# Performance work log

Hardware: AMD Instinct MI355X
Metric: run time of the kernel (lower is better)

## Reference

```python
import jax, jax.numpy as jnp
import numpy as np

DIM = 96
HEADS = 6
WS = 8                      # window_size
OWS = int(WS * 0.5) + WS    # overlap_win_size = 12
PAD = (OWS - WS) // 2       # 2
Dd = Hh = Ww = 24
B = 1
L = Dd * Hh * Ww
MLP_H = DIM * 2
TBL = (WS + OWS - 1) ** 3   # 6859 relative-position-bias entries


def setup_inputs() -> dict:
    key = jax.random.key(0)
    ks = jax.random.split(key, 8)
    def n(k, shape, s=0.02):
        return jax.random.normal(k, shape, jnp.float32) * s
    return {
        "x": jax.random.normal(ks[0], (B, L, DIM), jnp.float32),
        "ln1_w": jnp.ones((DIM,), jnp.float32),
        "ln1_b": jnp.zeros((DIM,), jnp.float32),
        "qkv_w": n(ks[1], (3 * DIM, DIM)),
        "qkv_b": jnp.zeros((3 * DIM,), jnp.float32),
        "rpb": n(ks[2], (TBL, HEADS)),
        "proj_w": n(ks[3], (DIM, DIM)),
        "proj_b": jnp.zeros((DIM,), jnp.float32),
        "ln2_w": jnp.ones((DIM,), jnp.float32),
        "ln2_b": jnp.zeros((DIM,), jnp.float32),
        "fc1_w": n(ks[4], (MLP_H, DIM)),
        "fc1_b": jnp.zeros((MLP_H,), jnp.float32),
        "fc2_w": n(ks[5], (DIM, MLP_H)),
        "fc2_b": jnp.zeros((DIM,), jnp.float32),
        "rpi": jax.random.randint(ks[6], (WS ** 3, OWS ** 3), 0, TBL),
        "D": Dd, "H": Hh, "W": Ww,
    }


def _ln(x, w, b):
    m = jnp.mean(x, -1, keepdims=True)
    v = jnp.var(x, -1, keepdims=True)
    return (x - m) / jnp.sqrt(v + 1e-5) * w + b


def _ocab3d(x, ln1_w, ln1_b, qkv_w, qkv_b, rpb, proj_w, proj_b,
            ln2_w, ln2_b, fc1_w, fc1_b, fc2_w, fc2_b, rpi, D, H, W):
    Bz, Lz, C = x.shape
    hd = C // HEADS
    scale = hd ** -0.5
    shortcut = x

    xn = _ln(x, ln1_w, ln1_b).reshape(Bz, D, H, W, C)
    qkv = xn @ qkv_w.T + qkv_b                   # [B,D,H,W,3C]
    q = qkv[..., :C]
    kv = qkv[..., C:]                            # cat(k, v) on channels, [B,D,H,W,2C]

    nD, nH, nW = D // WS, H // WS, W // WS
    nw = nD * nH * nW

    # non-overlapping query windows -> [B*nw, WS^3, C]
    qw = q.reshape(Bz, nD, WS, nH, WS, nW, WS, C)
    qw = qw.transpose(0, 1, 3, 5, 2, 4, 6, 7).reshape(Bz * nw, WS ** 3, C)

    # overlapping kv windows via pad + strided gather (mirrors F.pad + unfold)
    kvp = jnp.pad(kv, ((0, 0), (PAD, PAD), (PAD, PAD), (PAD, PAD), (0, 0)))
    idx_d = (jnp.arange(nD) * WS)[:, None] + jnp.arange(OWS)[None, :]
    idx_h = (jnp.arange(nH) * WS)[:, None] + jnp.arange(OWS)[None, :]
    idx_w = (jnp.arange(nW) * WS)[:, None] + jnp.arange(OWS)[None, :]
    kw = kvp[:, idx_d]                 # [B,nD,OWS,Hp,Wp,2C]
    kw = kw[:, :, :, idx_h]            # [B,nD,OWS,nH,OWS,Wp,2C]
    kw = kw[:, :, :, :, :, idx_w]      # [B,nD,OWS,nH,OWS,nW,OWS,2C]
    kw = kw.transpose(0, 1, 3, 5, 2, 4, 6, 7).reshape(Bz * nw, OWS ** 3, 2 * C)
    kk, vv = kw[..., :C], kw[..., C:]

    qh = qw.reshape(-1, WS ** 3, HEADS, hd).transpose(0, 2, 1, 3) * scale
    kh = kk.reshape(-1, OWS ** 3, HEADS, hd).transpose(0, 2, 1, 3)
    vh = vv.reshape(-1, OWS ** 3, HEADS, hd).transpose(0, 2, 1, 3)

    attn = jnp.einsum('bhqd,bhkd->bhqk', qh, kh)               # [B*nw,H,512,1728]
    bias = rpb[rpi.reshape(-1)].reshape(WS ** 3, OWS ** 3, HEADS).transpose(2, 0, 1)
    attn = jax.nn.softmax(attn + bias[None], axis=-1)
    out = jnp.einsum('bhqk,bhkd->bhqd', attn, vh)
    out = out.transpose(0, 2, 1, 3).reshape(Bz * nw, WS ** 3, C)

    # window reverse -> [B, L, C]
    out = out.reshape(Bz, nD, nH, nW, WS, WS, WS, C)
    out = out.transpose(0, 1, 4, 2, 5, 3, 6, 7).reshape(Bz, D * H * W, C)

    x2 = out @ proj_w.T + proj_b + shortcut
    h1 = jax.nn.gelu(_ln(x2, ln2_w, ln2_b) @ fc1_w.T + fc1_b, approximate=False)
    return x2 + (h1 @ fc2_w.T + fc2_b)


def reference(x, ln1_w, ln1_b, qkv_w, qkv_b, rpb, proj_w, proj_b,
              ln2_w, ln2_b, fc1_w, fc1_b, fc2_w, fc2_b, rpi, D, H, W):
    return _ocab3d(x, ln1_w, ln1_b, qkv_w, qkv_b, rpb, proj_w, proj_b,
                   ln2_w, ln2_b, fc1_w, fc1_b, fc2_w, fc2_b, rpi, D, H, W)
```

## Files before the change

kernel.cpp:

```cpp
#include <hip/hip_runtime.h>
#include <math.h>

#define DIMC   96
#define NHEADS 6
#define HD     16
#define WSZ    8
#define OWSZ   12
#define PADW   2
#define DD     24
#define LTOK   13824
#define NWIN   27
#define NKEY   1728
#define NROW   512
#define MLPH   192
#define PDIM   28
#define PD3    21952
#define TBL    6859
#define LSTR   82944
#define AOSTR  1327104
#define LOG2E  1.4426950408889634f

typedef __attribute__((ext_vector_type(4))) short bf16x4;
typedef __attribute__((ext_vector_type(8))) short bf16x8;
typedef __attribute__((ext_vector_type(4))) float f32x4;

__device__ __forceinline__ unsigned short bfround(float f) {
    unsigned u = __float_as_uint(f);
    return (unsigned short)((u + 0x7FFFu + ((u >> 16) & 1u)) >> 16);
}
__device__ __forceinline__ unsigned bfpack(float a, float b) {
    unsigned ua = __float_as_uint(a), ub = __float_as_uint(b);
    ua = (ua + 0x7FFFu + ((ua >> 16) & 1u)) >> 16;
    ub = (ub + 0x7FFFu + ((ub >> 16) & 1u)) >> 16;
    return ua | (ub << 16);
}
__device__ __forceinline__ uint4 pack8(const float* v) {
    uint4 u;
    u.x = bfpack(v[0], v[1]); u.y = bfpack(v[2], v[3]);
    u.z = bfpack(v[4], v[5]); u.w = bfpack(v[6], v[7]);
    return u;
}
__device__ __forceinline__ bf16x4 pack4(f32x4 p) {
    union { uint2 u; bf16x4 v; } r;
    r.u.x = __builtin_amdgcn_perm(__float_as_uint(p[1]), __float_as_uint(p[0]), 0x07060302u);
    r.u.y = __builtin_amdgcn_perm(__float_as_uint(p[3]), __float_as_uint(p[2]), 0x07060302u);
    return r.v;
}
__device__ __forceinline__ f32x4 mfma16(bf16x4 a, bf16x4 b, f32x4 c) {
#if __has_builtin(__builtin_amdgcn_mfma_f32_16x16x16bf16_1k)
    return __builtin_amdgcn_mfma_f32_16x16x16bf16_1k(a, b, c, 0, 0, 0);
#else
    bf16x8 a8 = {a[0], a[1], a[2], a[3], 0, 0, 0, 0};
    bf16x8 b8 = {b[0], b[1], b[2], b[3], 0, 0, 0, 0};
    return __builtin_amdgcn_mfma_f32_16x16x32_bf16(a8, b8, c, 0, 0, 0);
#endif
}
__device__ __forceinline__ float fexp2(float x) {
#if __has_builtin(__builtin_amdgcn_exp2f)
    return __builtin_amdgcn_exp2f(x);
#else
    return exp2f(x);
#endif
}

#define QKVB 1296
#define ZB   515
#define WPB  45
#define BIASB 216
__global__ __launch_bounds__(256) void qkvz_kernel(
        const float* __restrict__ X, const float* __restrict__ W,
        const float* __restrict__ bias, const float* __restrict__ lnw,
        const float* __restrict__ lnb,
        const float* __restrict__ projw, const float* __restrict__ fc1w,
        const float* __restrict__ fc2w,
        const int* __restrict__ rpi, const float* __restrict__ rpb,
        unsigned short* __restrict__ q16, unsigned short* __restrict__ kvp2,
        uint4* __restrict__ wpack, float* __restrict__ biasP) {
    __shared__ uint4 Af4[2 * 3 * 4 * 16];
    __shared__ uint4 Bf4[6 * 3 * 4 * 16];
    int bx = blockIdx.x, tid = threadIdx.x;

    if (bx >= QKVB + ZB + WPB) {
        int b2 = bx - (QKVB + ZB + WPB);
        int kt = b2 >> 1, qh = b2 & 1;
        int k0 = kt * 16;
        int qi = qh * 256 + tid;
        const int* rp = rpi + (long)qi * NKEY + k0;
        int idx[16];
        #pragma unroll
        for (int j = 0; j < 4; ++j) {
            int4 t = *(const int4*)(rp + j * 4);
            idx[j*4+0] = t.x * NHEADS; idx[j*4+1] = t.y * NHEADS;
            idx[j*4+2] = t.z * NHEADS; idx[j*4+3] = t.w * NHEADS;
        }
        #pragma unroll
        for (int head = 0; head < NHEADS; ++head) {
            #pragma unroll
            for (int quad = 0; quad < 4; ++quad) {
                float4 v;
                v.x = rpb[idx[quad*4+0] + head] * LOG2E;
                v.y = rpb[idx[quad*4+1] + head] * LOG2E;
                v.z = rpb[idx[quad*4+2] + head] * LOG2E;
                v.w = rpb[idx[quad*4+3] + head] * LOG2E;
                *(float4*)(biasP + ((((long)head*108 + kt)*4 + quad)*512 + qi)*4) = v;
            }
        }
        return;
    }
    if (bx >= QKVB + ZB) {
        int u = (bx - QKVB - ZB) * 256 + tid;
        if (u < 5760) {
            int p = (u < 1152) ? u : (u < 3456 ? (u - 1152) % 1152 : (u - 3456) % 1152);
            int nn = p & 15, r = p >> 4, qg = r & 3, r2 = r >> 2;
            int kt = r2 % 3, ct = r2 / 3;
            int n = ct * 16 + nn, g = kt * 4 + qg;
            const float* src;
            if (u < 1152)      src = projw + n * 96 + g * 8;
            else if (u < 3456) { int nc = (u - 1152) / 1152; src = fc1w + (long)(nc * 96 + n) * 96 + g * 8; }
            else               { int kh = (u - 3456) / 1152; src = fc2w + (long)n * 192 + kh * 96 + g * 8; }
            const float4* s4 = (const float4*)src;
            float v[8];
            float4 t0 = s4[0], t1 = s4[1];
            v[0]=t0.x; v[1]=t0.y; v[2]=t0.z; v[3]=t0.w;
            v[4]=t1.x; v[5]=t1.y; v[6]=t1.z; v[7]=t1.w;
            wpack[u] = pack8(v);
        }
        return;
    }
    if (bx >= QKVB) {
        int t = (bx - QKVB) * 256 + tid;
        if (t < 21952 * 6) {
            int head = t / PD3, pos = t % PD3;
            int d = pos / 784, h = (pos / 28) % 28, w = pos % 28;
            if (d < 2 || d >= 26 || h < 2 || h >= 26 || w < 2 || w >= 26) {
                uint4* p = (uint4*)(kvp2 + ((long)head * PD3 + pos) * 32);
                uint4 z = make_uint4(0, 0, 0, 0);
                p[0] = z; p[1] = z; p[2] = z; p[3] = z;
            }
        }
        return;
    }

    int nc   = bx % 3;
    int row0 = (bx / 3) * 32;

    if (tid < 128) {
        int row = tid >> 2, part = tid & 3;
        int rt = row >> 4, mm = row & 15;
        float v[24];
        const float4* xp = (const float4*)(X + (long)(row0 + row) * 96 + part * 24);
        float s = 0.f, sq = 0.f;
        #pragma unroll
        for (int i = 0; i < 6; ++i) {
            float4 t = xp[i];
            v[i*4+0] = t.x; v[i*4+1] = t.y; v[i*4+2] = t.z; v[i*4+3] = t.w;
            s  += t.x + t.y + t.z + t.w;
            sq += t.x*t.x + t.y*t.y + t.z*t.z + t.w*t.w;
        }
        s  += __shfl_xor(s, 1);  s  += __shfl_xor(s, 2);
        sq += __shfl_xor(sq, 1); sq += __shfl_xor(sq, 2);
        float mean = s * (1.f / 96.f);
        float inv  = rsqrtf(sq * (1.f / 96.f) - mean * mean + 1e-5f);
        const float4* wp = (const float4*)(lnw + part * 24);
        const float4* bp = (const float4*)(lnb + part * 24);
        #pragma unroll
        for (int i = 0; i < 6; ++i) {
            float4 wv = wp[i], bv = bp[i];
            v[i*4+0] = (v[i*4+0] - mean) * inv * wv.x + bv.x;
            v[i*4+1] = (v[i*4+1] - mean) * inv * wv.y + bv.y;
            v[i*4+2] = (v[i*4+2] - mean) * inv * wv.z + bv.z;
            v[i*4+3] = (v[i*4+3] - mean) * inv * wv.w + bv.w;
        }
        #pragma unroll
        for (int gg = 0; gg < 3; ++gg) {
            int g = part * 3 + gg;
            int kt = g >> 2, qq = g & 3;
            Af4[((rt * 3 + kt) * 4 + qq) * 16 + mm] = pack8(v + gg * 8);
        }
    }
    for (int idx = tid; idx < 96 * 12; idx += 256) {
        int n = idx / 12;
        int g = idx % 12;
        const float4* wp = (const float4*)(W + (long)(nc * 96 + n) * 96 + g * 8);
        float v[8];
        float4 t0 = wp[0], t1 = wp[1];
        v[0]=t0.x; v[1]=t0.y; v[2]=t0.z; v[3]=t0.w;
        v[4]=t1.x; v[5]=t1.y; v[6]=t1.z; v[7]=t1.w;
        int ct = n >> 4, nn = n & 15, kt = g >> 2, qg = g & 3;
        Bf4[((ct * 3 + kt) * 4 + qg) * 16 + nn] = pack8(v);
    }
    __syncthreads();

    int wave = tid >> 6, lane = tid & 63;
    int qq = lane >> 4, mI = lane & 15;
    int rt = wave & 1, cg = wave >> 1;

    f32x4 acc[3];
    #pragma unroll
    for (int j = 0; j < 3; ++j) acc[j] = (f32x4){0.f, 0.f, 0.f, 0.f};
    #pragma unroll
    for (int kt = 0; kt < 3; ++kt) {
        bf16x8 a = *(const bf16x8*)&Af4[((rt * 3 + kt) * 4 + qq) * 16 + mI];
        #pragma unroll
        for (int j = 0; j < 3; ++j) {
            bf16x8 b = *(const bf16x8*)&Bf4[(((cg * 3 + j) * 3 + kt) * 4 + qq) * 16 + mI];
            acc[j] = __builtin_amdgcn_mfma_f32_16x16x32_bf16(a, b, acc[j], 0, 0, 0);
        }
    }

    float bv[3];
    #pragma unroll
    for (int j = 0; j < 3; ++j) bv[j] = bias[nc * 96 + (cg * 3 + j) * 16 + mI];
    #pragma unroll
    for (int r = 0; r < 4; ++r) {
        int row = row0 + rt * 16 + qq * 4 + r;
        if (nc == 0) {
            unsigned short* op = q16 + (long)row * 96;
            #pragma unroll
            for (int j = 0; j < 3; ++j)
                op[(cg * 3 + j) * 16 + mI] = bfround(0.25f * LOG2E * (acc[j][r] + bv[j]));
        } else {
            int d = row / 576, hh = (row / 24) % 24, w2 = row % 24;
            long pos = ((long)(d + 2) * 28 + (hh + 2)) * 28 + (w2 + 2);
            #pragma unroll
            for (int j = 0; j < 3; ++j) {
                int head = cg * 3 + j;
                kvp2[((long)head * PD3 + pos) * 32 +
                     (nc == 2 ? 16 : 0) + mI] = bfround(acc[j][r] + bv[j]);
            }
        }
    }
}

#define KSTR 20
#define VST2 22
__global__ __launch_bounds__(256) void attn_kernel(
        const unsigned short* __restrict__ q, const unsigned short* __restrict__ kvp2,
        const float* __restrict__ biasP, float* __restrict__ ao,
        float* __restrict__ lbuf) {
    __shared__ unsigned short Ks[2][64 * KSTR];
    __shared__ unsigned short Vs[2][64 * VST2];
    int bid = blockIdx.x;
    int w = bid / 48, rem = bid % 48;
    int head = rem >> 3;
    int quart = (rem >> 1) & 3, half = rem & 1;
    int wd8 = (w / 9) * 8, wh8 = ((w / 3) % 3) * 8, ww8 = (w % 3) * 8;
    int tid = threadIdx.x, wave = tid >> 6, lane = tid & 63;
    int quad = lane >> 4, m16 = lane & 15;
    int key = tid >> 2, part = tid & 3;
    int c0 = half ? 13 : 0;
    int cn = half ? 14 : 13;

    auto kvaddr = [&](int c) -> const uint4* {
        int jg = c * 64 + key;
        int i = jg / 144, jh = (jg / 12) % 12, jw = jg % 12;
        long sp = ((long)(wd8 + i) * PDIM + (wh8 + jh)) * PDIM + (ww8 + jw);
        return (const uint4*)(kvp2 + ((long)head * PD3 + sp) * 32 + part * 8);
    };
    auto writeLDS = [&](int b, uint4 v) {
        if (part < 2) {
            *(uint2*)(&Ks[b][key * KSTR + part * 8])     = make_uint2(v.x, v.y);
            *(uint2*)(&Ks[b][key * KSTR + part * 8 + 4]) = make_uint2(v.z, v.w);
        } else {
            int d0 = (part - 2) * 8;
            *(uint2*)(&Vs[b][key * VST2 + d0])     = make_uint2(v.x, v.y);
            *(uint2*)(&Vs[b][key * VST2 + d0 + 4]) = make_uint2(v.z, v.w);
        }
    };

    bf16x4 qf[2];
    #pragma unroll
    for (int qt = 0; qt < 2; ++qt) {
        int ql = quart * 128 + wave * 32 + qt * 16 + m16;
        int ld = ql >> 6, lh = (ql >> 3) & 7, lw = ql & 7;
        int g = ((wd8 + ld) * 24 + (wh8 + lh)) * 24 + (ww8 + lw);
        qf[qt] = *(const bf16x4*)(q + (long)g * 96 + head * 16 + quad * 4);
    }

    const float* bbase = biasP + (long)head * 884736 + quad * 2048
                         + ((quart * 128 + wave * 32 + m16) << 2);
    f32x4 bcur[2][4];
    #pragma unroll
    for (int qt = 0; qt < 2; ++qt)
        #pragma unroll
        for (int kt = 0; kt < 4; ++kt)
            bcur[qt][kt] = *(const f32x4*)(bbase + (long)(c0*4 + kt) * 8192 + qt * 64);

    writeLDS(0, *kvaddr(c0));

    const bf16x4 onesf = {(short)0x3F80, (short)0x3F80, (short)0x3F80, (short)0x3F80};
    f32x4 o[2], lacc[2];
    o[0] = (f32x4){0.f,0.f,0.f,0.f}; o[1] = (f32x4){0.f,0.f,0.f,0.f};
    lacc[0] = o[0]; lacc[1] = o[1];
    uint4 stgn;

    #pragma unroll 1
    for (int cc = 0; cc < cn; ++cc) {
        int c = c0 + cc;
        if (cc + 1 < cn) stgn = *kvaddr(c + 1);
        __syncthreads();
        int b = cc & 1;

        bf16x4 kf[4];
        #pragma unroll
        for (int kt = 0; kt < 4; ++kt)
            kf[kt] = *(const bf16x4*)(&Ks[b][(kt * 16 + m16) * KSTR + quad * 4]);

        f32x4 S[2][4];
        #pragma unroll
        for (int qt = 0; qt < 2; ++qt)
            #pragma unroll
            for (int kt = 0; kt < 4; ++kt)
                S[qt][kt] = mfma16(kf[kt], qf[qt], bcur[qt][kt]);

        f32x4 bnxt[2][4];
        if (cc + 1 < cn) {
            const float* bp = bbase + (long)(c + 1) * 32768;
            #pragma unroll
            for (int qt = 0; qt < 2; ++qt)
                #pragma unroll
                for (int kt = 0; kt < 4; ++kt)
                    bnxt[qt][kt] = *(const f32x4*)(bp + kt * 8192 + qt * 64);
        }

        bf16x4 Pb[2][4];
        #pragma unroll
        for (int qt = 0; qt < 2; ++qt)
            #pragma unroll
            for (int kt = 0; kt < 4; ++kt) {
                f32x4 p;
                #pragma unroll
                for (int r = 0; r < 4; ++r) p[r] = fexp2(S[qt][kt][r]);
                Pb[qt][kt] = pack4(p);
                lacc[qt] = mfma16(Pb[qt][kt], onesf, lacc[qt]);
            }

        #pragma unroll
        for (int kt = 0; kt < 4; ++kt) {
            union { unsigned short s[4]; bf16x4 v; } u;
            int base = (kt * 16 + quad * 4) * VST2 + m16;
            u.s[0] = Vs[b][base];
            u.s[1] = Vs[b][base + VST2];
            u.s[2] = Vs[b][base + 2 * VST2];
            u.s[3] = Vs[b][base + 3 * VST2];
            o[0] = mfma16(Pb[0][kt], u.v, o[0]);
            o[1] = mfma16(Pb[1][kt], u.v, o[1]);
        }

        if (cc + 1 < cn) writeLDS((cc + 1) & 1, stgn);
        #pragma unroll
        for (int qt = 0; qt < 2; ++qt)
            #pragma unroll
            for (int kt = 0; kt < 4; ++kt) bcur[qt][kt] = bnxt[qt][kt];
    }

    float* aout = ao + (long)half * AOSTR;
    float* lout = lbuf + (long)half * LSTR;
    #pragma unroll
    for (int qt = 0; qt < 2; ++qt) {
        #pragma unroll
        for (int r = 0; r < 4; ++r) {
            int ql = quart * 128 + wave * 32 + qt * 16 + quad * 4 + r;
            int ld = ql >> 6, lh = (ql >> 3) & 7, lw = ql & 7;
            int g = ((wd8 + ld) * 24 + (wh8 + lh)) * 24 + (ww8 + lw);
            aout[(long)g * 96 + head * 16 + m16] = o[qt][r];
            if (m16 == 0) lout[g * 6 + head] = lacc[qt][r];
        }
    }
}

#define X2S 100
__global__ __launch_bounds__(512) void mlp_kernel(
        const float* __restrict__ ao0, const float* __restrict__ ao1,
        const float* __restrict__ lbuf, const uint4* __restrict__ wpack,
        const float* __restrict__ projb, const float* __restrict__ x,
        const float* __restrict__ ln2w, const float* __restrict__ ln2b,
        const float* __restrict__ fc1b, const float* __restrict__ fc2b,
        float* __restrict__ out) {
    __shared__ uint4 Ws[5760];
    __shared__ uint4 Af4[4 * 3 * 4 * 16];
    __shared__ float x2s[64 * X2S];
    __shared__ unsigned short h16[64 * 192];
    int tid = threadIdx.x;
    int row0 = blockIdx.x * 64;
    int wave = tid >> 6, lane = tid & 63;
    int qq = lane >> 4, mI = lane & 15;
    int rt = wave & 3, cg = wave >> 2;

    for (int idx = tid; idx < 5760; idx += 512) Ws[idx] = wpack[idx];

    if (tid < 256) {
        int row = tid >> 2, part = tid & 3;
        int rtA = row >> 4, mm = row & 15;
        int grow = row0 + row;
        const float4* a0 = (const float4*)(ao0 + (long)grow * 96 + part * 24);
        const float4* a1 = (const float4*)(ao1 + (long)grow * 96 + part * 24);
        int ha = (part * 3) >> 1, hb = ha + 1;
        float inva = 1.f / (lbuf[grow*6 + ha] + lbuf[LSTR + grow*6 + ha]);
        float invb = 1.f / (lbuf[grow*6 + hb] + lbuf[LSTR + grow*6 + hb]);
        float v[24];
        #pragma unroll
        for (int i = 0; i < 6; ++i) {
            float4 u0 = a0[i], u1 = a1[i];
            #pragma unroll
            for (int j = 0; j < 4; ++j) {
                int gc = part * 24 + i * 4 + j;
                float lv = ((gc >> 4) == ha) ? inva : invb;
                float s = (j==0?u0.x+u1.x : j==1?u0.y+u1.y : j==2?u0.z+u1.z : u0.w+u1.w);
                v[i*4+j] = s * lv;
            }
        }
        #pragma unroll
        for (int gg = 0; gg < 3; ++gg) {
            int g = part * 3 + gg;
            int kt = g >> 2, q4 = g & 3;
            Af4[((rtA * 3 + kt) * 4 + q4) * 16 + mm] = pack8(v + gg * 8);
        }
    }
    __syncthreads();

    {
        f32x4 acc[3];
        #pragma unroll
        for (int j = 0; j < 3; ++j) acc[j] = (f32x4){0.f,0.f,0.f,0.f};
        #pragma unroll
        for (int kt = 0; kt < 3; ++kt) {
            bf16x8 a = *(const bf16x8*)&Af4[((rt * 3 + kt) * 4 + qq) * 16 + mI];
            #pragma unroll
            for (int j = 0; j < 3; ++j) {
                bf16x8 b = *(const bf16x8*)&Ws[(((cg * 3 + j) * 3 + kt) * 4 + qq) * 16 + mI];
                acc[j] = __builtin_amdgcn_mfma_f32_16x16x32_bf16(a, b, acc[j], 0, 0, 0);
            }
        }
        float bv[3];
        #pragma unroll
        for (int j = 0; j < 3; ++j) bv[j] = projb[(cg * 3 + j) * 16 + mI];
        #pragma unroll
        for (int r = 0; r < 4; ++r) {
            int row = rt * 16 + qq * 4 + r;
            int grow = row0 + row;
            #pragma unroll
            for (int j = 0; j < 3; ++j) {
                int col = (cg * 3 + j) * 16 + mI;
                x2s[row * X2S + col] = acc[j][r] + bv[j] + x[(long)grow * 96 + col];
            }
        }
    }
    __syncthreads();

    if (tid < 256) {
        int row = tid >> 2, part = tid & 3;
        int rtA = row >> 4, mm = row & 15;
        float v[24];
        const float4* xp = (const float4*)(x2s + row * X2S + part * 24);
        float s = 0.f, sq = 0.f;
        #pragma unroll
        for (int i = 0; i < 6; ++i) {
            float4 t = xp[i];
            v[i*4+0] = t.x; v[i*4+1] = t.y; v[i*4+2] = t.z; v[i*4+3] = t.w;
            s  += t.x + t.y + t.z + t.w;
            sq += t.x*t.x + t.y*t.y + t.z*t.z + t.w*t.w;
        }
        s  += __shfl_xor(s, 1);  s  += __shfl_xor(s, 2);
        sq += __shfl_xor(sq, 1); sq += __shfl_xor(sq, 2);
        float mean = s * (1.f / 96.f);
        float inv  = rsqrtf(sq * (1.f / 96.f) - mean * mean + 1e-5f);
        const float4* wp = (const float4*)(ln2w + part * 24);
        const float4* bp = (const float4*)(ln2b + part * 24);
        #pragma unroll
        for (int i = 0; i < 6; ++i) {
            float4 wv = wp[i], bv = bp[i];
            v[i*4+0] = (v[i*4+0] - mean) * inv * wv.x + bv.x;
            v[i*4+1] = (v[i*4+1] - mean) * inv * wv.y + bv.y;
            v[i*4+2] = (v[i*4+2] - mean) * inv * wv.z + bv.z;
            v[i*4+3] = (v[i*4+3] - mean) * inv * wv.w + bv.w;
        }
        #pragma unroll
        for (int gg = 0; gg < 3; ++gg) {
            int g = part * 3 + gg;
            int kt = g >> 2, q4 = g & 3;
            Af4[((rtA * 3 + kt) * 4 + q4) * 16 + mm] = pack8(v + gg * 8);
        }
    }
    __syncthreads();

    #pragma unroll
    for (int nc = 0; nc < 2; ++nc) {
        f32x4 acc[3];
        #pragma unroll
        for (int j = 0; j < 3; ++j) acc[j] = (f32x4){0.f,0.f,0.f,0.f};
        #pragma unroll
        for (int kt = 0; kt < 3; ++kt) {
            bf16x8 a = *(const bf16x8*)&Af4[((rt * 3 + kt) * 4 + qq) * 16 + mI];
            #pragma unroll
            for (int j = 0; j < 3; ++j) {
                bf16x8 b = *(const bf16x8*)&Ws[1152 + nc * 1152 +
                               (((cg * 3 + j) * 3 + kt) * 4 + qq) * 16 + mI];
                acc[j] = __builtin_amdgcn_mfma_f32_16x16x32_bf16(a, b, acc[j], 0, 0, 0);
            }
        }
        float bv[3];
        #pragma unroll
        for (int j = 0; j < 3; ++j) bv[j] = fc1b[nc * 96 + (cg * 3 + j) * 16 + mI];
        #pragma unroll
        for (int r = 0; r < 4; ++r) {
            int row = rt * 16 + qq * 4 + r;
            #pragma unroll
            for (int j = 0; j < 3; ++j) {
                int col = nc * 96 + (cg * 3 + j) * 16 + mI;
                float v = acc[j][r] + bv[j];
                float g = 0.5f * v * (1.f + erff(v * 0.70710678f));
                int fi = (((row >> 4) * 6 + (col >> 5)) * 4 + ((col >> 3) & 3)) * 16 + (row & 15);
                h16[fi * 8 + (col & 7)] = bfround(g);
            }
        }
    }
    __syncthreads();

    f32x4 acc2[3];
    #pragma unroll
    for (int j = 0; j < 3; ++j) acc2[j] = (f32x4){0.f,0.f,0.f,0.f};
    #pragma unroll
    for (int kh = 0; kh < 2; ++kh) {
        #pragma unroll
        for (int kt = 0; kt < 3; ++kt) {
            int ktA = kh * 3 + kt;
            bf16x8 a = *(const bf16x8*)&h16[(((rt * 6 + ktA) * 4 + qq) * 16 + mI) * 8];
            #pragma unroll
            for (int j = 0; j < 3; ++j) {
                bf16x8 b = *(const bf16x8*)&Ws[3456 + kh * 1152 +
                               (((cg * 3 + j) * 3 + kt) * 4 + qq) * 16 + mI];
                acc2[j] = __builtin_amdgcn_mfma_f32_16x16x32_bf16(a, b, acc2[j], 0, 0, 0);
            }
        }
    }
    float bv[3];
    #pragma unroll
    for (int j = 0; j < 3; ++j) bv[j] = fc2b[(cg * 3 + j) * 16 + mI];
    #pragma unroll
    for (int r = 0; r < 4; ++r) {
        int row = rt * 16 + qq * 4 + r;
        int grow = row0 + row;
        #pragma unroll
        for (int j = 0; j < 3; ++j) {
            int col = (cg * 3 + j) * 16 + mI;
            out[(long)grow * 96 + col] = acc2[j][r] + bv[j] + x2s[row * X2S + col];
        }
    }
}

extern "C" void kernel_launch(void* const* d_in, const int* in_sizes, int n_in,
                              void* d_out, int out_size, void* d_ws, size_t ws_size,
                              hipStream_t stream) {
    const float* x     = (const float*)d_in[0];
    const float* ln1w  = (const float*)d_in[1];
    const float* ln1b  = (const float*)d_in[2];
    const float* qkvw  = (const float*)d_in[3];
    const float* qkvb  = (const float*)d_in[4];
    const float* rpb   = (const float*)d_in[5];
    const float* projw = (const float*)d_in[6];
    const float* projb = (const float*)d_in[7];
    const float* ln2w  = (const float*)d_in[8];
    const float* ln2b  = (const float*)d_in[9];
    const float* fc1w  = (const float*)d_in[10];
    const float* fc1b  = (const float*)d_in[11];
    const float* fc2w  = (const float*)d_in[12];
    const float* fc2b  = (const float*)d_in[13];
    const int*   rpi   = (const int*)d_in[14];
    float* outp = (float*)d_out;

    float* ws = (float*)d_ws;
    float*          aop    = ws;
    unsigned short* q16    = (unsigned short*)(ws + 2654208);
    unsigned short* kvp16  = (unsigned short*)(ws + 3317760);
    float*          biasPf = ws + 5425152;
    float*          lbuf   = ws + 10733568;
    uint4*          wpack  = (uint4*)(ws + 10899456);

    qkvz_kernel<<<QKVB + ZB + WPB + BIASB, 256, 0, stream>>>(
        x, qkvw, qkvb, ln1w, ln1b, projw, fc1w, fc2w, rpi, rpb,
        q16, kvp16, wpack, biasPf);
    attn_kernel<<<NWIN * NHEADS * 4 * 2, 256, 0, stream>>>(q16, kvp16, biasPf, aop, lbuf);
    mlp_kernel<<<LTOK / 64, 512, 0, stream>>>(aop, aop + AOSTR, lbuf, wpack, projb, x,
                                              ln2w, ln2b, fc1b, fc2b, outp);
}
```

Baseline: 170.2 us.

## Store bias table in bf16 and use K=32 MFMA in attention loop

The precomputed relative-position bias table is now stored as bf16 instead of fp32, which halves the bias bytes the attention kernel streams per key chunk. The bias-build blocks are regrouped so each thread writes head pairs from a float2 read of the rpb table. The attention loop is unrolled by two with ping-pong buffers so the double-buffer copy disappears, and it uses the 16x16x32 bf16 MFMA with a permuted key order to halve the P·V and row-sum MFMA count. Launch bounds now request 3 blocks per CU. The cost is bias precision reduced to bf16 and extra unpacking arithmetic in the inner loop.

```diff
diff --git a/kernel.cpp b/kernel.cpp
--- a/kernel.cpp
+++ b/kernel.cpp
@@ -46,6 +46,14 @@
     r.u.y = __builtin_amdgcn_perm(__float_as_uint(p[3]), __float_as_uint(p[2]), 0x07060302u);
     return r.v;
 }
+__device__ __forceinline__ f32x4 cvt4(uint2 b) {
+    f32x4 c;
+    c[0] = __uint_as_float(b.x << 16);
+    c[1] = __uint_as_float(b.x & 0xffff0000u);
+    c[2] = __uint_as_float(b.y << 16);
+    c[3] = __uint_as_float(b.y & 0xffff0000u);
+    return c;
+}
 __device__ __forceinline__ f32x4 mfma16(bf16x4 a, bf16x4 b, f32x4 c) {
 #if __has_builtin(__builtin_amdgcn_mfma_f32_16x16x16bf16_1k)
     return __builtin_amdgcn_mfma_f32_16x16x16bf16_1k(a, b, c, 0, 0, 0);
@@ -54,6 +62,9 @@
     bf16x8 b8 = {b[0], b[1], b[2], b[3], 0, 0, 0, 0};
     return __builtin_amdgcn_mfma_f32_16x16x32_bf16(a8, b8, c, 0, 0, 0);
 #endif
+}
+__device__ __forceinline__ f32x4 mfma32k(bf16x8 a, bf16x8 b, f32x4 c) {
+    return __builtin_amdgcn_mfma_f32_16x16x32_bf16(a, b, c, 0, 0, 0);
 }
 __device__ __forceinline__ float fexp2(float x) {
 #if __has_builtin(__builtin_amdgcn_exp2f)
@@ -75,34 +86,35 @@
         const float* __restrict__ fc2w,
         const int* __restrict__ rpi, const float* __restrict__ rpb,
         unsigned short* __restrict__ q16, unsigned short* __restrict__ kvp2,
-        uint4* __restrict__ wpack, float* __restrict__ biasP) {
+        uint4* __restrict__ wpack, unsigned short* __restrict__ biasP) {
     __shared__ uint4 Af4[2 * 3 * 4 * 16];
     __shared__ uint4 Bf4[6 * 3 * 4 * 16];
     int bx = blockIdx.x, tid = threadIdx.x;
 
     if (bx >= QKVB + ZB + WPB) {
         int b2 = bx - (QKVB + ZB + WPB);
-        int kt = b2 >> 1, qh = b2 & 1;
-        int k0 = kt * 16;
+        int g = b2 >> 1, qh = b2 & 1;
         int qi = qh * 256 + tid;
-        const int* rp = rpi + (long)qi * NKEY + k0;
-        int idx[16];
-        #pragma unroll
-        for (int j = 0; j < 4; ++j) {
-            int4 t = *(const int4*)(rp + j * 4);
-            idx[j*4+0] = t.x * NHEADS; idx[j*4+1] = t.y * NHEADS;
-            idx[j*4+2] = t.z * NHEADS; idx[j*4+3] = t.w * NHEADS;
-        }
-        #pragma unroll
-        for (int head = 0; head < NHEADS; ++head) {
-            #pragma unroll
-            for (int quad = 0; quad < 4; ++quad) {
-                float4 v;
-                v.x = rpb[idx[quad*4+0] + head] * LOG2E;
-                v.y = rpb[idx[quad*4+1] + head] * LOG2E;
-                v.z = rpb[idx[quad*4+2] + head] * LOG2E;
-                v.w = rpb[idx[quad*4+3] + head] * LOG2E;
-                *(float4*)(biasP + ((((long)head*108 + kt)*4 + quad)*512 + qi)*4) = v;
+        const int* rp = rpi + (long)qi * NKEY + (g >> 2) * 64
+                        + ((g >> 1) & 1) * 32 + (g & 1) * 4;
+        #pragma unroll
+        for (int quadj = 0; quadj < 4; ++quadj) {
+            int4 t = *(const int4*)(rp + quadj * 8);
+            const float2* p0 = (const float2*)(rpb + (long)t.x * 6);
+            const float2* p1 = (const float2*)(rpb + (long)t.y * 6);
+            const float2* p2 = (const float2*)(rpb + (long)t.z * 6);
+            const float2* p3 = (const float2*)(rpb + (long)t.w * 6);
+            unsigned short* oq = biasP + ((long)(g * 4 + quadj) * 512 + qi) * 4;
+            #pragma unroll
+            for (int hp = 0; hp < 3; ++hp) {
+                float2 a0 = p0[hp], a1 = p1[hp], a2 = p2[hp], a3 = p3[hp];
+                uint2 ua, ub;
+                ua.x = bfpack(a0.x * LOG2E, a1.x * LOG2E);
+                ua.y = bfpack(a2.x * LOG2E, a3.x * LOG2E);
+                ub.x = bfpack(a0.y * LOG2E, a1.y * LOG2E);
+                ub.y = bfpack(a2.y * LOG2E, a3.y * LOG2E);
+                *(uint2*)(oq + (long)(hp * 2)     * 884736) = ua;
+                *(uint2*)(oq + (long)(hp * 2 + 1) * 884736) = ub;
             }
         }
         return;
@@ -234,9 +246,66 @@
 
 #define KSTR 20
 #define VST2 22
-__global__ __launch_bounds__(256) void attn_kernel(
+
+#define ATTN_STEP(P, BCUR, BNXT)                                              \
+    {                                                                         \
+        int c = c0 + cc + (P);                                                \
+        bool more = (cc + (P) + 1 < cn);                                      \
+        if (more) stgn = *kvaddr(c + 1);                                      \
+        __syncthreads();                                                      \
+        bf16x4 kf[4];                                                         \
+        kf[0] = *(const bf16x4*)&Ks[(P)][kfO];                                \
+        kf[1] = *(const bf16x4*)&Ks[(P)][kfO + 4 * KSTR];                     \
+        kf[2] = *(const bf16x4*)&Ks[(P)][kfO + 32 * KSTR];                    \
+        kf[3] = *(const bf16x4*)&Ks[(P)][kfO + 36 * KSTR];                    \
+        f32x4 S[2][4];                                                        \
+        _Pragma("unroll")                                                     \
+        for (int qt = 0; qt < 2; ++qt) {                                      \
+            _Pragma("unroll")                                                 \
+            for (int kt = 0; kt < 4; ++kt)                                    \
+                S[qt][kt] = mfma16(kf[kt], qf[qt], cvt4(BCUR[qt][kt]));       \
+        }                                                                     \
+        if (more) {                                                           \
+            const unsigned short* bp = bbase + (long)(c + 1) * 32768;         \
+            _Pragma("unroll")                                                 \
+            for (int qt = 0; qt < 2; ++qt) {                                  \
+                _Pragma("unroll")                                             \
+                for (int kt = 0; kt < 4; ++kt)                                \
+                    BNXT[qt][kt] = *(const uint2*)(bp + kt * 8192 + qt * 64); \
+            }                                                                 \
+        }                                                                     \
+        bf16x8 P8[2][2];                                                      \
+        _Pragma("unroll")                                                     \
+        for (int qt = 0; qt < 2; ++qt) {                                      \
+            _Pragma("unroll")                                                 \
+            for (int u = 0; u < 2; ++u) {                                     \
+                f32x4 p0, p1;                                                 \
+                _Pragma("unroll")                                             \
+                for (int r = 0; r < 4; ++r) {                                 \
+                    p0[r] = fexp2(S[qt][2 * u][r]);                           \
+                    p1[r] = fexp2(S[qt][2 * u + 1][r]);                       \
+                }                                                             \
+                union { struct { bf16x4 lo, hi; } h; bf16x8 v; } uu;          \
+                uu.h.lo = pack4(p0); uu.h.hi = pack4(p1);                     \
+                P8[qt][u] = uu.v;                                             \
+                lacc[qt] = mfma32k(P8[qt][u], ones8, lacc[qt]);               \
+            }                                                                 \
+        }                                                                     \
+        _Pragma("unroll")                                                     \
+        for (int u = 0; u < 2; ++u) {                                         \
+            union { unsigned short s[8]; bf16x8 v; } vb;                      \
+            int vbase = (u * 32 + quad * 8) * VST2 + m16;                     \
+            _Pragma("unroll")                                                 \
+            for (int i = 0; i < 8; ++i) vb.s[i] = Vs[(P)][vbase + i * VST2];  \
+            o[0] = mfma32k(P8[0][u], vb.v, o[0]);                             \
+            o[1] = mfma32k(P8[1][u], vb.v, o[1]);                             \
+        }                                                                     \
+        if (more) writeLDS((P) ^ 1, stgn);                                    \
+    }
+
+__global__ __launch_bounds__(256, 3) void attn_kernel(
         const unsigned short* __restrict__ q, const unsigned short* __restrict__ kvp2,
-        const float* __restrict__ biasP, float* __restrict__ ao,
+        const unsigned short* __restrict__ biasP, float* __restrict__ ao,
         float* __restrict__ lbuf) {
     __shared__ unsigned short Ks[2][64 * KSTR];
     __shared__ unsigned short Vs[2][64 * VST2];
@@ -277,81 +346,29 @@
         qf[qt] = *(const bf16x4*)(q + (long)g * 96 + head * 16 + quad * 4);
     }
 
-    const float* bbase = biasP + (long)head * 884736 + quad * 2048
+    const unsigned short* bbase = biasP + (long)head * 884736 + quad * 2048
                          + ((quart * 128 + wave * 32 + m16) << 2);
-    f32x4 bcur[2][4];
+    uint2 bb0[2][4], bb1[2][4];
     #pragma unroll
     for (int qt = 0; qt < 2; ++qt)
         #pragma unroll
         for (int kt = 0; kt < 4; ++kt)
-            bcur[qt][kt] = *(const f32x4*)(bbase + (long)(c0*4 + kt) * 8192 + qt * 64);
+            bb0[qt][kt] = *(const uint2*)(bbase + (long)(c0 * 4 + kt) * 8192 + qt * 64);
 
     writeLDS(0, *kvaddr(c0));
 
-    const bf16x4 onesf = {(short)0x3F80, (short)0x3F80, (short)0x3F80, (short)0x3F80};
+    int kfO = ((m16 >> 2) * 8 + (m16 & 3)) * KSTR + quad * 4;
+
+    const bf16x8 ones8 = {(short)0x3F80, (short)0x3F80, (short)0x3F80, (short)0x3F80,
+                          (short)0x3F80, (short)0x3F80, (short)0x3F80, (short)0x3F80};
     f32x4 o[2], lacc[2];
     o[0] = (f32x4){0.f,0.f,0.f,0.f}; o[1] = (f32x4){0.f,0.f,0.f,0.f};
     lacc[0] = o[0]; lacc[1] = o[1];
     uint4 stgn;
 
-    #pragma unroll 1
-    for (int cc = 0; cc < cn; ++cc) {
-        int c = c0 + cc;
-        if (cc + 1 < cn) stgn = *kvaddr(c + 1);
-        __syncthreads();
-        int b = cc & 1;
-
-        bf16x4 kf[4];
-        #pragma unroll
-        for (int kt = 0; kt < 4; ++kt)
-            kf[kt] = *(const bf16x4*)(&Ks[b][(kt * 16 + m16) * KSTR + quad * 4]);
-
-        f32x4 S[2][4];
-        #pragma unroll
-        for (int qt = 0; qt < 2; ++qt)
-            #pragma unroll
-            for (int kt = 0; kt < 4; ++kt)
-                S[qt][kt] = mfma16(kf[kt], qf[qt], bcur[qt][kt]);
-
-        f32x4 bnxt[2][4];
-        if (cc + 1 < cn) {
-            const float* bp = bbase + (long)(c + 1) * 32768;
-            #pragma unroll
-            for (int qt = 0; qt < 2; ++qt)
-                #pragma unroll
-                for (int kt = 0; kt < 4; ++kt)
-                    bnxt[qt][kt] = *(const f32x4*)(bp + kt * 8192 + qt * 64);
-        }
-
-        bf16x4 Pb[2][4];
-        #pragma unroll
-        for (int qt = 0; qt < 2; ++qt)
-            #pragma unroll
-            for (int kt = 0; kt < 4; ++kt) {
-                f32x4 p;
-                #pragma unroll
-                for (int r = 0; r < 4; ++r) p[r] = fexp2(S[qt][kt][r]);
-                Pb[qt][kt] = pack4(p);
-                lacc[qt] = mfma16(Pb[qt][kt], onesf, lacc[qt]);
-            }
-
-        #pragma unroll
-        for (int kt = 0; kt < 4; ++kt) {
-            union { unsigned short s[4]; bf16x4 v; } u;
-            int base = (kt * 16 + quad * 4) * VST2 + m16;
-            u.s[0] = Vs[b][base];
-            u.s[1] = Vs[b][base + VST2];
-            u.s[2] = Vs[b][base + 2 * VST2];
-            u.s[3] = Vs[b][base + 3 * VST2];
-            o[0] = mfma16(Pb[0][kt], u.v, o[0]);
-            o[1] = mfma16(Pb[1][kt], u.v, o[1]);
-        }
-
-        if (cc + 1 < cn) writeLDS((cc + 1) & 1, stgn);
-        #pragma unroll
-        for (int qt = 0; qt < 2; ++qt)
-            #pragma unroll
-            for (int kt = 0; kt < 4; ++kt) bcur[qt][kt] = bnxt[qt][kt];
+    for (int cc = 0; cc < cn; cc += 2) {
+        ATTN_STEP(0, bb0, bb1)
+        if (cc + 1 < cn) ATTN_STEP(1, bb1, bb0)
     }
 
     float* aout = ao + (long)half * AOSTR;
@@ -573,14 +590,14 @@
     float*          aop    = ws;
     unsigned short* q16    = (unsigned short*)(ws + 2654208);
     unsigned short* kvp16  = (unsigned short*)(ws + 3317760);
-    float*          biasPf = ws + 5425152;
+    unsigned short* biasPh = (unsigned short*)(ws + 5425152);
     float*          lbuf   = ws + 10733568;
     uint4*          wpack  = (uint4*)(ws + 10899456);
 
     qkvz_kernel<<<QKVB + ZB + WPB + BIASB, 256, 0, stream>>>(
         x, qkvw, qkvb, ln1w, ln1b, projw, fc1w, fc2w, rpi, rpb,
-        q16, kvp16, wpack, biasPf);
-    attn_kernel<<<NWIN * NHEADS * 4 * 2, 256, 0, stream>>>(q16, kvp16, biasPf, aop, lbuf);
+        q16, kvp16, wpack, biasPh);
+    attn_kernel<<<NWIN * NHEADS * 4 * 2, 256, 0, stream>>>(q16, kvp16, biasPh, aop, lbuf);
     mlp_kernel<<<LTOK / 64, 512, 0, stream>>>(aop, aop + AOSTR, lbuf, wpack, projb, x,
                                               ln2w, ln2b, fc1b, fc2b, outp);
 }
```

Measured after the change: 162.5 us. 4.6% less time.
